# Kernel optimization log

Measured on AMD Instinct MI355X. Metric: run time of the kernel, lower is better.

Reference implementation:

```python
import jax, jax.numpy as jnp
import numpy as np

HIDDEN = 6      # tiny MLP width
GRID_R = 16     # CAM grid resolution
NUM_LAYERS = 2  # num hidden layers == shared_cam.num_layers
OUT_DIM = 3
N_POINTS = 2_097_152
LN_EPS = 1e-5


def _bilinear_border(grid, xy):
    """F.grid_sample(mode='bilinear', padding_mode='border', align_corners=True)
    for point queries. grid: [C, R, R]; xy: [N, 2] in [-1, 1] with xy[:,0]=x
    (width) and xy[:,1]=y (height). Returns [N, C]."""
    R = grid.shape[-1]
    # align_corners=True mapping to pixel coords, border padding = clamp
    coords = jnp.clip((xy + 1.0) * 0.5 * (R - 1), 0.0, float(R - 1))
    ix, iy = coords[:, 0], coords[:, 1]
    x0f, y0f = jnp.floor(ix), jnp.floor(iy)
    wx, wy = ix - x0f, iy - y0f                       # [N]
    x0 = x0f.astype(jnp.int32)
    y0 = y0f.astype(jnp.int32)
    x1 = jnp.minimum(x0 + 1, R - 1)
    y1 = jnp.minimum(y0 + 1, R - 1)
    g00 = grid[:, y0, x0]  # [C, N]
    g01 = grid[:, y0, x1]
    g10 = grid[:, y1, x0]
    g11 = grid[:, y1, x1]
    top = g00 * (1.0 - wx) + g01 * wx
    bot = g10 * (1.0 - wx) + g11 * wx
    return (top * (1.0 - wy) + bot * wy).T            # [N, C]


def _layernorm(h, w, b):
    mu = jnp.mean(h, axis=-1, keepdims=True)
    var = jnp.mean((h - mu) ** 2, axis=-1, keepdims=True)  # biased, like torch LN
    return (h - mu) * jax.lax.rsqrt(var + LN_EPS) * w + b


def setup_inputs() -> dict:
    key = jax.random.key(0)
    ks = jax.random.split(key, 10)
    xy = jax.random.uniform(ks[0], (N_POINTS, 2), dtype=jnp.float32,
                            minval=-1.0, maxval=1.0)
    # CAM grids (init is ones/zeros; perturb so the math is exercised)
    gamma = 1.0 + 0.1 * jax.random.normal(ks[1], (NUM_LAYERS, HIDDEN, GRID_R, GRID_R), jnp.float32)
    beta = 0.1 * jax.random.normal(ks[2], (NUM_LAYERS, HIDDEN, GRID_R, GRID_R), jnp.float32)
    # Tiny MLP weights (Kaiming-ish scale)
    w_in = jax.random.normal(ks[3], (HIDDEN, 2), jnp.float32) / np.sqrt(2.0)
    b_in = 0.1 * jax.random.normal(ks[4], (HIDDEN,), jnp.float32)
    w_h = jax.random.normal(ks[5], (NUM_LAYERS - 1, HIDDEN, HIDDEN), jnp.float32) / np.sqrt(HIDDEN)
    b_h = 0.1 * jax.random.normal(ks[6], (NUM_LAYERS - 1, HIDDEN), jnp.float32)
    w_out = jax.random.normal(ks[7], (OUT_DIM, HIDDEN), jnp.float32) / np.sqrt(HIDDEN)
    b_out = 0.1 * jax.random.normal(ks[8], (OUT_DIM,), jnp.float32)
    ln_w = 1.0 + 0.05 * jax.random.normal(ks[9], (NUM_LAYERS, HIDDEN), jnp.float32)
    ln_b = jnp.zeros((NUM_LAYERS, HIDDEN), jnp.float32)
    return {"xy": xy, "gamma": gamma, "beta": beta, "w_in": w_in, "b_in": b_in,
            "w_h": w_h, "b_h": b_h, "w_out": w_out, "b_out": b_out,
            "ln_w": ln_w, "ln_b": ln_b}


def reference(xy, gamma, beta, w_in, b_in, w_h, b_h, w_out, b_out, ln_w, ln_b):
    # h = act(in_layer(xy))
    h = jax.nn.silu(xy @ w_in.T + b_in)                    # [N, HIDDEN]
    for i in range(NUM_LAYERS):
        if i > 0:
            h = jax.nn.silu(h @ w_h[i - 1].T + b_h[i - 1])
        g = _bilinear_border(gamma[i], xy)                 # [N, HIDDEN]
        bb = _bilinear_border(beta[i], xy)                 # [N, HIDDEN]
        h = g * _layernorm(h, ln_w[i], ln_b[i]) + bb
    return h @ w_out.T + b_out                             # [N, OUT_DIM]
```

## Files before the change

kernel.cpp:

```cpp
#include <hip/hip_runtime.h>
#include <hip/hip_fp16.h>
#include <stdint.h>

#define NPTS 2097152
#define BLOCK 256
#define PPT 4
#define NBLK (NPTS / (BLOCK * PPT))

static __device__ __forceinline__ float silu_f(float v) {
    return v * __builtin_amdgcn_rcpf(1.0f + __expf(-v));
}
static __device__ __forceinline__ __half2 u2h(uint32_t u) {
    union { uint32_t i; __half2 h; } v; v.i = u; return v.h;
}
static __device__ __forceinline__ uint32_t h2u(__half2 h) {
    union { __half2 h; uint32_t i; } v; v.h = h; return v.i;
}

__global__ __launch_bounds__(BLOCK, 4) void camfield_kernel(
    const float* __restrict__ xy,
    const float* __restrict__ gamma,
    const float* __restrict__ beta,
    const float* __restrict__ w_in,
    const float* __restrict__ b_in,
    const float* __restrict__ w_h,
    const float* __restrict__ b_h,
    const float* __restrict__ w_out,
    const float* __restrict__ b_out,
    const float* __restrict__ ln_w,
    const float* __restrict__ ln_b,
    float* __restrict__ out)
{
    __shared__ __align__(16) uint32_t sg[2][256][12];

    const int tid = threadIdx.x;

    for (int idx = tid; idx < 3072; idx += BLOCK) {
        int l = (idx >= 1536) ? 1 : 0;
        int r = idx - l * 1536;
        int s = r >> 8;
        int cell = r & 255;
        int x = cell & 15;
        int x1 = (x < 15) ? x + 1 : 15;
        int rowb = cell - x;
        const float* src = (s < 3) ? (gamma + l * 1536 + (2 * s) * 256)
                                   : (beta  + l * 1536 + (2 * (s - 3)) * 256);
        float a_lo = src[rowb + x];
        float a_hi = src[256 + rowb + x];
        float b_lo = src[rowb + x1];
        float b_hi = src[256 + rowb + x1];
        sg[l][cell][2 * s]     = h2u(__floats2half2_rn(a_lo, a_hi));
        sg[l][cell][2 * s + 1] = h2u(__floats2half2_rn(b_lo, b_hi));
    }

    float Win0[6], Win1[6], Bin[6], Wh[6][6], Bh[6], Wo[3][6], Bo[3], LnW[2][6], LnB[2][6];
#pragma unroll
    for (int j = 0; j < 6; ++j) {
        Win0[j] = w_in[2 * j];
        Win1[j] = w_in[2 * j + 1];
        Bin[j]  = b_in[j];
        Bh[j]   = b_h[j];
#pragma unroll
        for (int k = 0; k < 6; ++k) Wh[j][k] = w_h[6 * j + k];
        LnW[0][j] = ln_w[j];     LnW[1][j] = ln_w[6 + j];
        LnB[0][j] = ln_b[j];     LnB[1][j] = ln_b[6 + j];
    }
#pragma unroll
    for (int j = 0; j < 3; ++j) {
        Bo[j] = b_out[j];
#pragma unroll
        for (int k = 0; k < 6; ++k) Wo[j][k] = w_out[6 * j + k];
    }

    __syncthreads();

    const int p0 = (blockIdx.x * BLOCK + tid) * PPT;

    const float4* xv = (const float4*)(xy + 2 * p0);
    float4 q0 = xv[0];
    float4 q1 = xv[1];
    float xs[4] = { q0.x, q0.z, q1.x, q1.z };
    float ys[4] = { q0.y, q0.w, q1.y, q1.w };

    float o[3 * PPT];

#pragma unroll
    for (int p = 0; p < PPT; ++p) {
        const float x = xs[p];
        const float y = ys[p];

        float fx = fminf(fmaxf(fmaf(x, 7.5f, 7.5f), 0.0f), 15.0f);
        float fy = fminf(fmaxf(fmaf(y, 7.5f, 7.5f), 0.0f), 15.0f);
        int x0 = (int)fx; if (x0 > 14) x0 = 14;
        int y0 = (int)fy; if (y0 > 14) y0 = 14;
        float wx = fx - (float)x0;
        float wy = fy - (float)y0;
        float w11f = wx * wy;
        float w10f = wy - w11f;
        float w01f = wx - w11f;
        float w00f = 1.0f - wx - wy + w11f;

        const __half2 W00 = __float2half2_rn(w00f);
        const __half2 W01 = __float2half2_rn(w01f);
        const __half2 W10 = __float2half2_rn(w10f);
        const __half2 W11 = __float2half2_rn(w11f);

        const int cell = (y0 << 4) + x0;

        float gl[2][6], bl[2][6];
#pragma unroll
        for (int l = 0; l < 2; ++l) {
            const uint4* c4 = (const uint4*)&sg[l][cell][0];
            uint4 u0 = c4[0];
            uint4 u1 = c4[1];
            uint4 u2 = c4[2];
            uint4 v0 = c4[48];
            uint4 v1 = c4[49];
            uint4 v2 = c4[50];

            uint32_t A[6] = { u0.x, u0.z, u1.x, u1.z, u2.x, u2.z };
            uint32_t B[6] = { u0.y, u0.w, u1.y, u1.w, u2.y, u2.w };
            uint32_t C[6] = { v0.x, v0.z, v1.x, v1.z, v2.x, v2.z };
            uint32_t D[6] = { v0.y, v0.w, v1.y, v1.w, v2.y, v2.w };

            float2 r[6];
#pragma unroll
            for (int s = 0; s < 6; ++s) {
                __half2 acc = __hmul2(u2h(A[s]), W00);
                acc = __hfma2(u2h(B[s]), W01, acc);
                acc = __hfma2(u2h(C[s]), W10, acc);
                acc = __hfma2(u2h(D[s]), W11, acc);
                r[s] = __half22float2(acc);
            }
            gl[l][0] = r[0].x; gl[l][1] = r[0].y;
            gl[l][2] = r[1].x; gl[l][3] = r[1].y;
            gl[l][4] = r[2].x; gl[l][5] = r[2].y;
            bl[l][0] = r[3].x; bl[l][1] = r[3].y;
            bl[l][2] = r[4].x; bl[l][3] = r[4].y;
            bl[l][4] = r[5].x; bl[l][5] = r[5].y;
        }

        float h[6];
#pragma unroll
        for (int j = 0; j < 6; ++j)
            h[j] = silu_f(fmaf(x, Win0[j], fmaf(y, Win1[j], Bin[j])));

        {
            float mu = (h[0] + h[1] + h[2] + h[3] + h[4] + h[5]) * (1.0f / 6.0f);
            float d[6], var = 0.0f;
#pragma unroll
            for (int j = 0; j < 6; ++j) { d[j] = h[j] - mu; var = fmaf(d[j], d[j], var); }
            var *= (1.0f / 6.0f);
            float rs = __builtin_amdgcn_rsqf(var + 1e-5f);
#pragma unroll
            for (int j = 0; j < 6; ++j)
                h[j] = fmaf(gl[0][j], fmaf(d[j] * rs, LnW[0][j], LnB[0][j]), bl[0][j]);
        }

        float t[6];
#pragma unroll
        for (int j = 0; j < 6; ++j) {
            float a = Bh[j];
#pragma unroll
            for (int k = 0; k < 6; ++k) a = fmaf(h[k], Wh[j][k], a);
            t[j] = silu_f(a);
        }

        {
            float mu = (t[0] + t[1] + t[2] + t[3] + t[4] + t[5]) * (1.0f / 6.0f);
            float d[6], var = 0.0f;
#pragma unroll
            for (int j = 0; j < 6; ++j) { d[j] = t[j] - mu; var = fmaf(d[j], d[j], var); }
            var *= (1.0f / 6.0f);
            float rs = __builtin_amdgcn_rsqf(var + 1e-5f);
#pragma unroll
            for (int j = 0; j < 6; ++j)
                t[j] = fmaf(gl[1][j], fmaf(d[j] * rs, LnW[1][j], LnB[1][j]), bl[1][j]);
        }

#pragma unroll
        for (int j = 0; j < 3; ++j) {
            float a = Bo[j];
#pragma unroll
            for (int k = 0; k < 6; ++k) a = fmaf(t[k], Wo[j][k], a);
            o[3 * p + j] = a;
        }
    }

    float4* op = (float4*)(out + 3 * p0);
#pragma unroll
    for (int q = 0; q < 3; ++q)
        op[q] = make_float4(o[4 * q], o[4 * q + 1], o[4 * q + 2], o[4 * q + 3]);
}

extern "C" void kernel_launch(void* const* d_in, const int* in_sizes, int n_in,
                              void* d_out, int out_size, void* d_ws, size_t ws_size,
                              hipStream_t stream) {
    camfield_kernel<<<NBLK, BLOCK, 0, stream>>>(
        (const float*)d_in[0],
        (const float*)d_in[1],
        (const float*)d_in[2],
        (const float*)d_in[3],
        (const float*)d_in[4],
        (const float*)d_in[5],
        (const float*)d_in[6],
        (const float*)d_in[7],
        (const float*)d_in[8],
        (const float*)d_in[9],
        (const float*)d_in[10],
        (float*)d_out);
}
```

Baseline: 109.7 us.

## Process two tiles per block, prefetch xy before LDS setup, fold LN weight into grid

```diff
diff --git a/kernel.cpp b/kernel.cpp
--- a/kernel.cpp
+++ b/kernel.cpp
@@ -5,7 +5,8 @@
 #define NPTS 2097152
 #define BLOCK 256
 #define PPT 4
-#define NBLK (NPTS / (BLOCK * PPT))
+#define TILES 2
+#define NBLK (NPTS / (BLOCK * PPT * TILES))
 
 static __device__ __forceinline__ float silu_f(float v) {
     return v * __builtin_amdgcn_rcpf(1.0f + __expf(-v));
@@ -34,6 +35,13 @@
     __shared__ __align__(16) uint32_t sg[2][256][12];
 
     const int tid = threadIdx.x;
+    const int blockBase = blockIdx.x * (BLOCK * PPT * TILES);
+    const int p0a = blockBase + tid * PPT;
+    const int p0b = blockBase + BLOCK * PPT + tid * PPT;
+
+    const float4* xva = (const float4*)(xy + 2 * p0a);
+    float4 qa0 = xva[0];
+    float4 qa1 = xva[1];
 
     for (int idx = tid; idx < 3072; idx += BLOCK) {
         int l = (idx >= 1536) ? 1 : 0;
@@ -43,17 +51,25 @@
         int x = cell & 15;
         int x1 = (x < 15) ? x + 1 : 15;
         int rowb = cell - x;
-        const float* src = (s < 3) ? (gamma + l * 1536 + (2 * s) * 256)
-                                   : (beta  + l * 1536 + (2 * (s - 3)) * 256);
-        float a_lo = src[rowb + x];
-        float a_hi = src[256 + rowb + x];
-        float b_lo = src[rowb + x1];
-        float b_hi = src[256 + rowb + x1];
+        const float* src;
+        float m_lo, m_hi;
+        if (s < 3) {
+            src = gamma + l * 1536 + (2 * s) * 256;
+            m_lo = ln_w[l * 6 + 2 * s];
+            m_hi = ln_w[l * 6 + 2 * s + 1];
+        } else {
+            src = beta + l * 1536 + (2 * (s - 3)) * 256;
+            m_lo = 1.0f; m_hi = 1.0f;
+        }
+        float a_lo = src[rowb + x] * m_lo;
+        float a_hi = src[256 + rowb + x] * m_hi;
+        float b_lo = src[rowb + x1] * m_lo;
+        float b_hi = src[256 + rowb + x1] * m_hi;
         sg[l][cell][2 * s]     = h2u(__floats2half2_rn(a_lo, a_hi));
         sg[l][cell][2 * s + 1] = h2u(__floats2half2_rn(b_lo, b_hi));
     }
 
-    float Win0[6], Win1[6], Bin[6], Wh[6][6], Bh[6], Wo[3][6], Bo[3], LnW[2][6], LnB[2][6];
+    float Win0[6], Win1[6], Bin[6], Wh[6][6], Bh[6], Wo[3][6], Bo[3], K[2][6];
 #pragma unroll
     for (int j = 0; j < 6; ++j) {
         Win0[j] = w_in[2 * j];
@@ -62,8 +78,8 @@
         Bh[j]   = b_h[j];
 #pragma unroll
         for (int k = 0; k < 6; ++k) Wh[j][k] = w_h[6 * j + k];
-        LnW[0][j] = ln_w[j];     LnW[1][j] = ln_w[6 + j];
-        LnB[0][j] = ln_b[j];     LnB[1][j] = ln_b[6 + j];
+        K[0][j] = ln_b[j] / ln_w[j];
+        K[1][j] = ln_b[6 + j] / ln_w[6 + j];
     }
 #pragma unroll
     for (int j = 0; j < 3; ++j) {
@@ -74,123 +90,126 @@
 
     __syncthreads();
 
-    const int p0 = (blockIdx.x * BLOCK + tid) * PPT;
-
-    const float4* xv = (const float4*)(xy + 2 * p0);
-    float4 q0 = xv[0];
-    float4 q1 = xv[1];
-    float xs[4] = { q0.x, q0.z, q1.x, q1.z };
-    float ys[4] = { q0.y, q0.w, q1.y, q1.w };
-
-    float o[3 * PPT];
-
-#pragma unroll
-    for (int p = 0; p < PPT; ++p) {
-        const float x = xs[p];
-        const float y = ys[p];
-
-        float fx = fminf(fmaxf(fmaf(x, 7.5f, 7.5f), 0.0f), 15.0f);
-        float fy = fminf(fmaxf(fmaf(y, 7.5f, 7.5f), 0.0f), 15.0f);
-        int x0 = (int)fx; if (x0 > 14) x0 = 14;
-        int y0 = (int)fy; if (y0 > 14) y0 = 14;
-        float wx = fx - (float)x0;
-        float wy = fy - (float)y0;
-        float w11f = wx * wy;
-        float w10f = wy - w11f;
-        float w01f = wx - w11f;
-        float w00f = 1.0f - wx - wy + w11f;
-
-        const __half2 W00 = __float2half2_rn(w00f);
-        const __half2 W01 = __float2half2_rn(w01f);
-        const __half2 W10 = __float2half2_rn(w10f);
-        const __half2 W11 = __float2half2_rn(w11f);
-
-        const int cell = (y0 << 4) + x0;
-
-        float gl[2][6], bl[2][6];
-#pragma unroll
-        for (int l = 0; l < 2; ++l) {
-            const uint4* c4 = (const uint4*)&sg[l][cell][0];
-            uint4 u0 = c4[0];
-            uint4 u1 = c4[1];
-            uint4 u2 = c4[2];
-            uint4 v0 = c4[48];
-            uint4 v1 = c4[49];
-            uint4 v2 = c4[50];
-
-            uint32_t A[6] = { u0.x, u0.z, u1.x, u1.z, u2.x, u2.z };
-            uint32_t B[6] = { u0.y, u0.w, u1.y, u1.w, u2.y, u2.w };
-            uint32_t C[6] = { v0.x, v0.z, v1.x, v1.z, v2.x, v2.z };
-            uint32_t D[6] = { v0.y, v0.w, v1.y, v1.w, v2.y, v2.w };
-
-            float2 r[6];
-#pragma unroll
-            for (int s = 0; s < 6; ++s) {
-                __half2 acc = __hmul2(u2h(A[s]), W00);
-                acc = __hfma2(u2h(B[s]), W01, acc);
-                acc = __hfma2(u2h(C[s]), W10, acc);
-                acc = __hfma2(u2h(D[s]), W11, acc);
-                r[s] = __half22float2(acc);
-            }
-            gl[l][0] = r[0].x; gl[l][1] = r[0].y;
-            gl[l][2] = r[1].x; gl[l][3] = r[1].y;
-            gl[l][4] = r[2].x; gl[l][5] = r[2].y;
-            bl[l][0] = r[3].x; bl[l][1] = r[3].y;
-            bl[l][2] = r[4].x; bl[l][3] = r[4].y;
-            bl[l][4] = r[5].x; bl[l][5] = r[5].y;
+    const float4* xvb = (const float4*)(xy + 2 * p0b);
+    float4 qb0 = xvb[0];
+    float4 qb1 = xvb[1];
+
+    auto process4 = [&](float4 Q0, float4 Q1, int p0) {
+        float xs[4] = { Q0.x, Q0.z, Q1.x, Q1.z };
+        float ys[4] = { Q0.y, Q0.w, Q1.y, Q1.w };
+        float o[3 * PPT];
+
+#pragma unroll
+        for (int p = 0; p < PPT; ++p) {
+            const float x = xs[p];
+            const float y = ys[p];
+
+            float fx = fminf(fmaxf(fmaf(x, 7.5f, 7.5f), 0.0f), 15.0f);
+            float fy = fminf(fmaxf(fmaf(y, 7.5f, 7.5f), 0.0f), 15.0f);
+            int x0 = (int)fx; if (x0 > 14) x0 = 14;
+            int y0 = (int)fy; if (y0 > 14) y0 = 14;
+            float wx = fx - (float)x0;
+            float wy = fy - (float)y0;
+            float w11f = wx * wy;
+            float w10f = wy - w11f;
+            float w01f = wx - w11f;
+            float w00f = 1.0f - wx - wy + w11f;
+
+            const __half2 W00 = __float2half2_rn(w00f);
+            const __half2 W01 = __float2half2_rn(w01f);
+            const __half2 W10 = __float2half2_rn(w10f);
+            const __half2 W11 = __float2half2_rn(w11f);
+
+            const int cell = (y0 << 4) + x0;
+
+            float gl[2][6], bl[2][6];
+#pragma unroll
+            for (int l = 0; l < 2; ++l) {
+                const uint4* c4 = (const uint4*)&sg[l][cell][0];
+                uint4 u0 = c4[0];
+                uint4 u1 = c4[1];
+                uint4 u2 = c4[2];
+                uint4 v0 = c4[48];
+                uint4 v1 = c4[49];
+                uint4 v2 = c4[50];
+
+                uint32_t A[6] = { u0.x, u0.z, u1.x, u1.z, u2.x, u2.z };
+                uint32_t B[6] = { u0.y, u0.w, u1.y, u1.w, u2.y, u2.w };
+                uint32_t C[6] = { v0.x, v0.z, v1.x, v1.z, v2.x, v2.z };
+                uint32_t D[6] = { v0.y, v0.w, v1.y, v1.w, v2.y, v2.w };
+
+                float2 r[6];
+#pragma unroll
+                for (int s = 0; s < 6; ++s) {
+                    __half2 acc = __hmul2(u2h(A[s]), W00);
+                    acc = __hfma2(u2h(B[s]), W01, acc);
+                    acc = __hfma2(u2h(C[s]), W10, acc);
+                    acc = __hfma2(u2h(D[s]), W11, acc);
+                    r[s] = __half22float2(acc);
+                }
+                gl[l][0] = r[0].x; gl[l][1] = r[0].y;
+                gl[l][2] = r[1].x; gl[l][3] = r[1].y;
+                gl[l][4] = r[2].x; gl[l][5] = r[2].y;
+                bl[l][0] = r[3].x; bl[l][1] = r[3].y;
+                bl[l][2] = r[4].x; bl[l][3] = r[4].y;
+                bl[l][4] = r[5].x; bl[l][5] = r[5].y;
+            }
+
+            float h[6];
+#pragma unroll
+            for (int j = 0; j < 6; ++j)
+                h[j] = silu_f(fmaf(x, Win0[j], fmaf(y, Win1[j], Bin[j])));
+
+            {
+                float mu = (h[0] + h[1] + h[2] + h[3] + h[4] + h[5]) * (1.0f / 6.0f);
+                float d[6], var = 0.0f;
+#pragma unroll
+                for (int j = 0; j < 6; ++j) { d[j] = h[j] - mu; var = fmaf(d[j], d[j], var); }
+                var *= (1.0f / 6.0f);
+                float rs = __builtin_amdgcn_rsqf(var + 1e-5f);
+#pragma unroll
+                for (int j = 0; j < 6; ++j)
+                    h[j] = fmaf(gl[0][j], fmaf(d[j], rs, K[0][j]), bl[0][j]);
+            }
+
+            float t[6];
+#pragma unroll
+            for (int j = 0; j < 6; ++j) {
+                float a = Bh[j];
+#pragma unroll
+                for (int k = 0; k < 6; ++k) a = fmaf(h[k], Wh[j][k], a);
+                t[j] = silu_f(a);
+            }
+
+            {
+                float mu = (t[0] + t[1] + t[2] + t[3] + t[4] + t[5]) * (1.0f / 6.0f);
+                float d[6], var = 0.0f;
+#pragma unroll
+                for (int j = 0; j < 6; ++j) { d[j] = t[j] - mu; var = fmaf(d[j], d[j], var); }
+                var *= (1.0f / 6.0f);
+                float rs = __builtin_amdgcn_rsqf(var + 1e-5f);
+#pragma unroll
+                for (int j = 0; j < 6; ++j)
+                    t[j] = fmaf(gl[1][j], fmaf(d[j], rs, K[1][j]), bl[1][j]);
+            }
+
+#pragma unroll
+            for (int j = 0; j < 3; ++j) {
+                float a = Bo[j];
+#pragma unroll
+                for (int k = 0; k < 6; ++k) a = fmaf(t[k], Wo[j][k], a);
+                o[3 * p + j] = a;
+            }
         }
 
-        float h[6];
-#pragma unroll
-        for (int j = 0; j < 6; ++j)
-            h[j] = silu_f(fmaf(x, Win0[j], fmaf(y, Win1[j], Bin[j])));
-
-        {
-            float mu = (h[0] + h[1] + h[2] + h[3] + h[4] + h[5]) * (1.0f / 6.0f);
-            float d[6], var = 0.0f;
-#pragma unroll
-            for (int j = 0; j < 6; ++j) { d[j] = h[j] - mu; var = fmaf(d[j], d[j], var); }
-            var *= (1.0f / 6.0f);
-            float rs = __builtin_amdgcn_rsqf(var + 1e-5f);
-#pragma unroll
-            for (int j = 0; j < 6; ++j)
-                h[j] = fmaf(gl[0][j], fmaf(d[j] * rs, LnW[0][j], LnB[0][j]), bl[0][j]);
-        }
-
-        float t[6];
-#pragma unroll
-        for (int j = 0; j < 6; ++j) {
-            float a = Bh[j];
-#pragma unroll
-            for (int k = 0; k < 6; ++k) a = fmaf(h[k], Wh[j][k], a);
-            t[j] = silu_f(a);
-        }
-
-        {
-            float mu = (t[0] + t[1] + t[2] + t[3] + t[4] + t[5]) * (1.0f / 6.0f);
-            float d[6], var = 0.0f;
-#pragma unroll
-            for (int j = 0; j < 6; ++j) { d[j] = t[j] - mu; var = fmaf(d[j], d[j], var); }
-            var *= (1.0f / 6.0f);
-            float rs = __builtin_amdgcn_rsqf(var + 1e-5f);
-#pragma unroll
-            for (int j = 0; j < 6; ++j)
-                t[j] = fmaf(gl[1][j], fmaf(d[j] * rs, LnW[1][j], LnB[1][j]), bl[1][j]);
-        }
-
-#pragma unroll
-        for (int j = 0; j < 3; ++j) {
-            float a = Bo[j];
-#pragma unroll
-            for (int k = 0; k < 6; ++k) a = fmaf(t[k], Wo[j][k], a);
-            o[3 * p + j] = a;
-        }
-    }
-
-    float4* op = (float4*)(out + 3 * p0);
-#pragma unroll
-    for (int q = 0; q < 3; ++q)
-        op[q] = make_float4(o[4 * q], o[4 * q + 1], o[4 * q + 2], o[4 * q + 3]);
+        float4* op = (float4*)(out + 3 * p0);
+#pragma unroll
+        for (int q = 0; q < 3; ++q)
+            op[q] = make_float4(o[4 * q], o[4 * q + 1], o[4 * q + 2], o[4 * q + 3]);
+    };
+
+    process4(qa0, qa1, p0a);
+    process4(qb0, qb1, p0b);
 }
 
 extern "C" void kernel_launch(void* const* d_in, const int* in_sizes, int n_in,
```

Result: slower. 113.2 us (+3.2%).
